# Kernel optimization log

Measured on AMD Instinct MI355X. Metric: run time of the kernel, lower is better.

## Reference

```python
import jax, jax.numpy as jnp
import numpy as np

LN2PI = float(np.log(2.0 * np.pi))
B, T, S = 256, 4096, 32


def setup_inputs() -> dict:
    key = jax.random.key(0)
    ks = jax.random.split(key, 6)
    obvs = jax.random.normal(ks[0], (B, T, 1), jnp.float32)
    ln_pi = jnp.ones((S,), jnp.float32) / S  # CategoricalPrior init: ones/num_states
    trans_w = 1.0 + 0.1 * jax.random.normal(ks[1], (S,), jnp.float32)  # diagonal
    trans_b = 0.1 * jax.random.normal(ks[2], (S,), jnp.float32)
    mu = jax.random.normal(ks[3], (S,), jnp.float32)
    log_sigma = 0.1 * jax.random.normal(ks[4], (S,), jnp.float32)
    return {"obvs": obvs, "ln_pi": ln_pi, "trans_w": trans_w,
            "trans_b": trans_b, "mu": mu, "log_sigma": log_sigma}


def reference(obvs, ln_pi, trans_w, trans_b, mu, log_sigma):
    # GaussianEmbedding: per-state Gaussian log-likelihood -> (B, T, S)
    z = (obvs - mu) * jnp.exp(-log_sigma)
    ln_e = -0.5 * z * z - log_sigma - 0.5 * LN2PI
    ln_e_t = jnp.swapaxes(ln_e, 0, 1)  # (T, B, S), time-major for scan

    # forward recurrence: f_t = emit_t + (w * f_{t-1} + b)
    f0 = ln_e_t[0] + ln_pi
    def fstep(carry, emit):
        nxt = emit + trans_w * carry + trans_b
        return nxt, nxt
    _, fs = jax.lax.scan(fstep, f0, ln_e_t[1:])
    ln_fs = jnp.concatenate([f0[None], fs], axis=0)  # (T, B, S)

    # backward recurrence: b_t = w * (b_{t+1} + emit_{t+1}) + b, b_{T-1} = emit_{T-1} + ln_pi
    bT = ln_e_t[-1] + ln_pi
    def bstep(carry, emit):
        nxt = trans_w * (carry + emit) + trans_b
        return nxt, nxt
    _, bs = jax.lax.scan(bstep, bT, ln_e_t[1:], reverse=True)  # bs[t] = b_t, t in [0, T-2]
    ln_bs = jnp.concatenate([bs, bT[None]], axis=0)  # (T, B, S)

    log_gamma = ln_fs + ln_bs
    log_gamma = log_gamma - jax.nn.logsumexp(log_gamma, axis=2, keepdims=True)
    return jnp.swapaxes(log_gamma, 0, 1)  # (B, T, S)
```

## Files before the change

kernel.cpp:

```cpp
#include <hip/hip_runtime.h>
#include <math.h>

constexpr int Bn = 256;
constexpr int Tn = 4096;
constexpr int Sn = 32;
constexpr int NE = 8;
constexpr int EL = Tn / NE;
constexpr int NT2 = 256;
constexpr int TCN = NT2 / Sn;
constexpr int TL = EL / TCN;
constexpr int CL = 16;
constexpr int CPT = TL / CL;
constexpr float HALF_LN2PI = 0.918938533204672742f;
constexpr float SAT = -3.0e38f;
constexpr float PCLAMP = 1.0e38f;

constexpr size_t OFF_LF = 0;
constexpr size_t OFF_LB = (size_t)Bn * NE * Sn;


#define DPP_ROR_ADD(x, ctrl) \
    ((x) + __int_as_float(__builtin_amdgcn_update_dpp(0, __float_as_int(x), (ctrl), 0xF, 0xF, false)))

__global__ __launch_bounds__(256) void hmm_agg_kernel(
    const float* __restrict__ obvs, const float* __restrict__ ln_pi,
    const float* __restrict__ trans_w, const float* __restrict__ trans_b,
    const float* __restrict__ mu, const float* __restrict__ log_sigma,
    float* __restrict__ ws)
{
    const int gid = blockIdx.x * 256 + threadIdx.x;
    const int s = gid & 31;
    const int e = (gid >> 5) & (NE - 1);
    const int b = gid >> 8;
    const float w  = trans_w[s];
    const float tb = trans_b[s];
    const float pi = ln_pi[s];
    const float m  = mu[s];
    const float ls = log_sigma[s];
    const float inv = __expf(-ls);
    const float cqa  = -0.5f * inv * inv;
    const float cqb  = m * inv * inv;
    const float cqcb = -ls - HALF_LN2PI - 0.5f * m * m * inv * inv + tb;
    const float tbb  = tb - w * tb;

    const float4* base = (const float4*)(obvs + (size_t)b * Tn + (size_t)e * EL);
    float a = 0.f, lb = 0.f;
#pragma unroll 4
    for (int j4 = 0; j4 < EL / 4; ++j4) {
        float4 x = base[j4];
        float4 y = base[EL / 4 - 1 - j4];
        float g0 = fmaf(fmaf(cqa, x.x, cqb), x.x, cqcb);
        float g1 = fmaf(fmaf(cqa, x.y, cqb), x.y, cqcb);
        float g2 = fmaf(fmaf(cqa, x.z, cqb), x.z, cqcb);
        float g3 = fmaf(fmaf(cqa, x.w, cqb), x.w, cqcb);
        if (e == 0 && j4 == 0) g0 += pi - tb;
        a = fmaf(w, a, g0);
        a = fmaf(w, a, g1);
        a = fmaf(w, a, g2);
        a = fmaf(w, a, g3);
        float d3 = fmaf(fmaf(cqa, y.w, cqb), y.w, cqcb);
        float d2 = fmaf(fmaf(cqa, y.z, cqb), y.z, cqcb);
        float d1 = fmaf(fmaf(cqa, y.y, cqb), y.y, cqcb);
        float d0 = fmaf(fmaf(cqa, y.x, cqb), y.x, cqcb);
        lb = fmaf(w, lb + d3, tbb);
        lb = fmaf(w, lb + d2, tbb);
        lb = fmaf(w, lb + d1, tbb);
        lb = fmaf(w, lb + d0, tbb);
    }
    ws[OFF_LF + (size_t)(b * NE + e) * Sn + s] = a;
    ws[OFF_LB + (size_t)(b * NE + e) * Sn + s] = lb;
}

__global__ __launch_bounds__(NT2, 8) void hmm_main_kernel(
    const float* __restrict__ obvs, const float* __restrict__ ln_pi,
    const float* __restrict__ trans_w, const float* __restrict__ trans_b,
    const float* __restrict__ mu, const float* __restrict__ log_sigma,
    float* __restrict__ out, const float* __restrict__ ws)
{
    __shared__ __align__(16) float s_obvs[EL];
    __shared__ float s_PF[TCN][Sn];
    __shared__ float s_ZB[TCN][Sn];
    __shared__ __align__(16) float s_tile[4][2][8][Sn];

    const int be  = blockIdx.x;
    const int b   = be >> 3;
    const int e   = be & (NE - 1);
    const int tid = threadIdx.x;
    const int s   = tid & 31;
    const int tc  = tid >> 5;
    const int wv  = tid >> 6;
    const int tcl = (tid >> 5) & 1;
    const int lane = tid & 63;
    const int t0  = tc * TL;

    if (tid < EL / 4)
        ((float4*)s_obvs)[tid] = ((const float4*)(obvs + (size_t)b * Tn + (size_t)e * EL))[tid];

    const float w  = trans_w[s];
    const float tb = trans_b[s];
    const float pi = ln_pi[s];
    const float m  = mu[s];
    const float ls = log_sigma[s];
    const float inv = __expf(-ls);
    const float cqa  = -0.5f * inv * inv;
    const float cqb  = m * inv * inv;
    const float cqcb = -ls - HALF_LN2PI - 0.5f * m * m * inv * inv + tb;
    const float tbb  = tb - w * tb;
    float w16; { float w2 = w * w, w4 = w2 * w2; float w8 = w4 * w4; w16 = w8 * w8; }
    const float W64 = fminf(fminf(w16 * w16, PCLAMP) * fminf(w16 * w16, PCLAMP), PCLAMP);
    const float l2w = log2f(w);
    const float WEL = fminf(exp2f(l2w * 512.0f), PCLAMP);
    const float pY  = fminf(exp2f(l2w * (float)(TL * tc)), PCLAMP);
    const float pX  = fminf(exp2f(l2w * (float)(TL * (7 - tc))), PCLAMP);
    const bool th0  = (e == 0) && (tc == 0);

    __syncthreads();

#define EMIT(xv) fmaf(fmaf(cqa, (xv), cqb), (xv), cqcb)

    float lbs[CPT];
    float AF = 0.f;
#pragma unroll
    for (int i = 0; i < CPT; ++i) {
        const float4* q4 = (const float4*)(s_obvs + t0 + i * CL);
        float4 v0 = q4[0], v1 = q4[1], v2 = q4[2], v3 = q4[3];
        float x[CL] = {v0.x, v0.y, v0.z, v0.w, v1.x, v1.y, v1.z, v1.w,
                       v2.x, v2.y, v2.z, v2.w, v3.x, v3.y, v3.z, v3.w};
#pragma unroll
        for (int j = 0; j < CL; ++j) {
            float g = EMIT(x[j]);
            if (th0 && i == 0 && j == 0) g += pi - tb;
            AF = fmaf(w, AF, g);
        }
        float l = 0.f;
#pragma unroll
        for (int j = CL - 2; j >= -1; --j)
            l = fmaf(w, l + EMIT(x[j + 1]), tbb);
        lbs[i] = l;
    }
    const float Z3 = lbs[3];
    const float Z2 = fmaf(w16, Z3, lbs[2]);
    const float Z1 = fmaf(w16, Z2, lbs[1]);
    const float ZT = fmaf(w16, Z1, lbs[0]);

    s_PF[tc][s] = AF;
    s_ZB[tc][s] = ZT;
    __syncthreads();

    {
        float Wd = W64;
#pragma unroll
        for (int r = 0; r < 3; ++r) {
            const int d = 1 << r;
            float tF = (tc >= d)      ? s_PF[tc - d][s] : 0.f;
            float tB = (tc + d < TCN) ? s_ZB[tc + d][s] : 0.f;
            __syncthreads();
            if (tc >= d)      s_PF[tc][s] = fmaf(Wd, tF, s_PF[tc][s]);
            if (tc + d < TCN) s_ZB[tc][s] = fmaf(Wd, tB, s_ZB[tc][s]);
            Wd = fminf(Wd * Wd, PCLAMP);
            __syncthreads();
        }
    }

    float Y = 0.f;
#pragma unroll
    for (int qq = 0; qq < NE - 1; ++qq)
        if (qq < e) Y = fmaf(WEL, Y, ws[OFF_LF + (size_t)(b * NE + qq) * Sn + s]);
    float xT = obvs[(size_t)b * Tn + Tn - 1];
    float X = EMIT(xT) + (pi - tb);
#pragma unroll
    for (int qq = NE - 1; qq > 0; --qq)
        if (qq > e) X = fmaf(WEL, X, ws[OFF_LB + (size_t)(b * NE + qq) * Sn + s]);

    const float Pprev  = (tc > 0)       ? s_PF[tc - 1][s] : 0.f;
    const float ZSnext = (tc < TCN - 1) ? s_ZB[tc + 1][s] : 0.f;
    float f         = fmaf(pY, Y, Pprev);
    const float Xth = fmaf(pX, X, ZSnext);
    float Rarr[CPT];
    Rarr[3] = Xth;
    {
        float p = w16;
        float Z = Z3;
        Rarr[2] = fmaf(p, Xth, Z);
        p = fminf(p * w16, PCLAMP); Z = Z2;
        Rarr[1] = fmaf(p, Xth, Z);
        p = fminf(p * w16, PCLAMP); Z = Z1;
        Rarr[0] = fmaf(p, Xth, Z);
    }

    const size_t rowbase = (size_t)b * Tn + (size_t)e * EL;
    const int qr  = lane & 7;
    const int t8r = (lane >> 3) & 7;

#pragma unroll
    for (int i = 0; i < CPT; ++i) {
        const float4* q4 = (const float4*)(s_obvs + t0 + i * CL);
        float4 v0 = q4[0], v1 = q4[1], v2 = q4[2], v3 = q4[3];
        float x[CL] = {v0.x, v0.y, v0.z, v0.w, v1.x, v1.y, v1.z, v1.w,
                       v2.x, v2.y, v2.z, v2.w, v3.x, v3.y, v3.z, v3.w};
        float barr[CL];
        barr[CL - 1] = Rarr[i];
#pragma unroll
        for (int j = CL - 2; j >= 0; --j)
            barr[j] = fmaf(w, barr[j + 1] + EMIT(x[j + 1]), tbb);

#pragma unroll
        for (int h = 0; h < 2; ++h) {
#pragma unroll
            for (int j8 = 0; j8 < 8; ++j8) {
                const int j = h * 8 + j8;
                float g = EMIT(x[j]);
                if (th0 && i == 0 && j == 0) g += pi - tb;
                f = fmaf(w, f, g);
                float v = f + barr[j];
                float sum = __expf(v);
                sum = DPP_ROR_ADD(sum, 0x121);
                sum = DPP_ROR_ADD(sum, 0x122);
                sum = DPP_ROR_ADD(sum, 0x124);
                sum = DPP_ROR_ADD(sum, 0x128);
                sum += __shfl_xor(sum, 16, 32);
                sum = fmaxf(sum, 1.0e-35f);
                s_tile[wv][tcl][j8][s] = fmaxf(v - __logf(sum), SAT);
            }
#pragma unroll
            for (int r2 = 0; r2 < 2; ++r2) {
                float4 val = *(const float4*)&s_tile[wv][r2][t8r][qr * 4];
                const int trow = (wv * 2 + r2) * TL + i * CL + h * 8 + t8r;
                *(float4*)(out + ((rowbase + trow) << 5) + qr * 4) = val;
            }
        }
    }
#undef EMIT
}

extern "C" void kernel_launch(void* const* d_in, const int* in_sizes, int n_in,
                              void* d_out, int out_size, void* d_ws, size_t ws_size,
                              hipStream_t stream)
{
    const float* obvs      = (const float*)d_in[0];
    const float* ln_pi     = (const float*)d_in[1];
    const float* trans_w   = (const float*)d_in[2];
    const float* trans_b   = (const float*)d_in[3];
    const float* mu        = (const float*)d_in[4];
    const float* log_sigma = (const float*)d_in[5];
    float* out = (float*)d_out;
    float* wsf = (float*)d_ws;

    hipLaunchKernelGGL(hmm_agg_kernel, dim3(Bn * NE * Sn / 256), dim3(256), 0, stream,
                       obvs, ln_pi, trans_w, trans_b, mu, log_sigma, wsf);
    hipLaunchKernelGGL(hmm_main_kernel, dim3(Bn * NE), dim3(NT2), 0, stream,
                       obvs, ln_pi, trans_w, trans_b, mu, log_sigma, out, wsf);
}
```

Measured before the change: 53.43 us.

## Precompute per-chunk scan prefixes in aggregate kernel and drop in-block scan

The aggregate kernel now also writes per-64-step forward prefix and backward suffix partials for each segment to the workspace. The main kernel reads them directly, which removes the shared-memory log-step scan and its barriers. Emissions are now computed once per element and reused by the forward and backward passes, and the cross-half-wave reduction uses permlane16_swap instead of a shuffle. The cost is more workspace traffic and stores in the first kernel, and the workspace must be large enough for the extra buffers.

After: 117.2 us. +119.4%, slower.

```diff
diff --git a/kernel.cpp b/kernel.cpp
--- a/kernel.cpp
+++ b/kernel.cpp
@@ -6,6 +6,7 @@
 constexpr int Sn = 32;
 constexpr int NE = 8;
 constexpr int EL = Tn / NE;
+constexpr int WPE = 8;
 constexpr int NT2 = 256;
 constexpr int TCN = NT2 / Sn;
 constexpr int TL = EL / TCN;
@@ -17,6 +18,8 @@
 
 constexpr size_t OFF_LF = 0;
 constexpr size_t OFF_LB = (size_t)Bn * NE * Sn;
+constexpr size_t OFF_PF = OFF_LB + (size_t)Bn * NE * Sn;
+constexpr size_t OFF_SB = OFF_PF + (size_t)Bn * NE * 7 * Sn;
 
 
 #define DPP_ROR_ADD(x, ctrl) \
@@ -45,27 +48,35 @@
 
     const float4* base = (const float4*)(obvs + (size_t)b * Tn + (size_t)e * EL);
     float a = 0.f, lb = 0.f;
-#pragma unroll 4
-    for (int j4 = 0; j4 < EL / 4; ++j4) {
-        float4 x = base[j4];
-        float4 y = base[EL / 4 - 1 - j4];
-        float g0 = fmaf(fmaf(cqa, x.x, cqb), x.x, cqcb);
-        float g1 = fmaf(fmaf(cqa, x.y, cqb), x.y, cqcb);
-        float g2 = fmaf(fmaf(cqa, x.z, cqb), x.z, cqcb);
-        float g3 = fmaf(fmaf(cqa, x.w, cqb), x.w, cqcb);
-        if (e == 0 && j4 == 0) g0 += pi - tb;
-        a = fmaf(w, a, g0);
-        a = fmaf(w, a, g1);
-        a = fmaf(w, a, g2);
-        a = fmaf(w, a, g3);
-        float d3 = fmaf(fmaf(cqa, y.w, cqb), y.w, cqcb);
-        float d2 = fmaf(fmaf(cqa, y.z, cqb), y.z, cqcb);
-        float d1 = fmaf(fmaf(cqa, y.y, cqb), y.y, cqcb);
-        float d0 = fmaf(fmaf(cqa, y.x, cqb), y.x, cqcb);
-        lb = fmaf(w, lb + d3, tbb);
-        lb = fmaf(w, lb + d2, tbb);
-        lb = fmaf(w, lb + d1, tbb);
-        lb = fmaf(w, lb + d0, tbb);
+#pragma unroll 1
+    for (int k = 0; k < WPE; ++k) {
+        const int kk = WPE - 1 - k;
+#pragma unroll 2
+        for (int j4 = 0; j4 < 16; ++j4) {
+            float4 x = base[k * 16 + j4];
+            float4 y = base[kk * 16 + (15 - j4)];
+            float g0 = fmaf(fmaf(cqa, x.x, cqb), x.x, cqcb);
+            float g1 = fmaf(fmaf(cqa, x.y, cqb), x.y, cqcb);
+            float g2 = fmaf(fmaf(cqa, x.z, cqb), x.z, cqcb);
+            float g3 = fmaf(fmaf(cqa, x.w, cqb), x.w, cqcb);
+            if (e == 0 && k == 0 && j4 == 0) g0 += pi - tb;
+            a = fmaf(w, a, g0);
+            a = fmaf(w, a, g1);
+            a = fmaf(w, a, g2);
+            a = fmaf(w, a, g3);
+            float d3 = fmaf(fmaf(cqa, y.w, cqb), y.w, cqcb);
+            float d2 = fmaf(fmaf(cqa, y.z, cqb), y.z, cqcb);
+            float d1 = fmaf(fmaf(cqa, y.y, cqb), y.y, cqcb);
+            float d0 = fmaf(fmaf(cqa, y.x, cqb), y.x, cqcb);
+            lb = fmaf(w, lb + d3, tbb);
+            lb = fmaf(w, lb + d2, tbb);
+            lb = fmaf(w, lb + d1, tbb);
+            lb = fmaf(w, lb + d0, tbb);
+        }
+        if (k < WPE - 1) {
+            ws[OFF_PF + ((size_t)(b * NE + e) * 7 + k) * Sn + s] = a;
+            ws[OFF_SB + ((size_t)(b * NE + e) * 7 + (kk - 1)) * Sn + s] = lb;
+        }
     }
     ws[OFF_LF + (size_t)(b * NE + e) * Sn + s] = a;
     ws[OFF_LB + (size_t)(b * NE + e) * Sn + s] = lb;
@@ -78,8 +89,6 @@
     float* __restrict__ out, const float* __restrict__ ws)
 {
     __shared__ __align__(16) float s_obvs[EL];
-    __shared__ float s_PF[TCN][Sn];
-    __shared__ float s_ZB[TCN][Sn];
     __shared__ __align__(16) float s_tile[4][2][8][Sn];
 
     const int be  = blockIdx.x;
@@ -107,7 +116,8 @@
     const float cqcb = -ls - HALF_LN2PI - 0.5f * m * m * inv * inv + tb;
     const float tbb  = tb - w * tb;
     float w16; { float w2 = w * w, w4 = w2 * w2; float w8 = w4 * w4; w16 = w8 * w8; }
-    const float W64 = fminf(fminf(w16 * w16, PCLAMP) * fminf(w16 * w16, PCLAMP), PCLAMP);
+    const float w32 = fminf(w16 * w16, PCLAMP);
+    const float w48 = fminf(w32 * w16, PCLAMP);
     const float l2w = log2f(w);
     const float WEL = fminf(exp2f(l2w * 512.0f), PCLAMP);
     const float pY  = fminf(exp2f(l2w * (float)(TL * tc)), PCLAMP);
@@ -118,8 +128,22 @@
 
 #define EMIT(xv) fmaf(fmaf(cqa, (xv), cqb), (xv), cqcb)
 
+    float Y = 0.f;
+#pragma unroll
+    for (int qq = 0; qq < NE - 1; ++qq)
+        if (qq < e) Y = fmaf(WEL, Y, ws[OFF_LF + (size_t)(b * NE + qq) * Sn + s]);
+    float xT = obvs[(size_t)b * Tn + Tn - 1];
+    float X = EMIT(xT) + (pi - tb);
+#pragma unroll
+    for (int qq = NE - 1; qq > 0; --qq)
+        if (qq > e) X = fmaf(WEL, X, ws[OFF_LB + (size_t)(b * NE + qq) * Sn + s]);
+
+    const float fprev = tc ? ws[OFF_PF + ((size_t)(b * NE + e) * 7 + (tc - 1)) * Sn + s] : 0.f;
+    float f = fmaf(pY, Y, fprev);
+    const float msuf = (tc < 7) ? ws[OFF_SB + ((size_t)(b * NE + e) * 7 + tc) * Sn + s] : 0.f;
+    const float Xth = fmaf(pX, X, msuf);
+
     float lbs[CPT];
-    float AF = 0.f;
 #pragma unroll
     for (int i = 0; i < CPT; ++i) {
         const float4* q4 = (const float4*)(s_obvs + t0 + i * CL);
@@ -127,66 +151,21 @@
         float x[CL] = {v0.x, v0.y, v0.z, v0.w, v1.x, v1.y, v1.z, v1.w,
                        v2.x, v2.y, v2.z, v2.w, v3.x, v3.y, v3.z, v3.w};
 #pragma unroll
-        for (int j = 0; j < CL; ++j) {
-            float g = EMIT(x[j]);
-            if (th0 && i == 0 && j == 0) g += pi - tb;
-            AF = fmaf(w, AF, g);
-        }
+        for (int j = 0; j < CL; ++j) x[j] = EMIT(x[j]);
         float l = 0.f;
 #pragma unroll
         for (int j = CL - 2; j >= -1; --j)
-            l = fmaf(w, l + EMIT(x[j + 1]), tbb);
+            l = fmaf(w, l + x[j + 1], tbb);
         lbs[i] = l;
     }
     const float Z3 = lbs[3];
     const float Z2 = fmaf(w16, Z3, lbs[2]);
     const float Z1 = fmaf(w16, Z2, lbs[1]);
-    const float ZT = fmaf(w16, Z1, lbs[0]);
-
-    s_PF[tc][s] = AF;
-    s_ZB[tc][s] = ZT;
-    __syncthreads();
-
-    {
-        float Wd = W64;
-#pragma unroll
-        for (int r = 0; r < 3; ++r) {
-            const int d = 1 << r;
-            float tF = (tc >= d)      ? s_PF[tc - d][s] : 0.f;
-            float tB = (tc + d < TCN) ? s_ZB[tc + d][s] : 0.f;
-            __syncthreads();
-            if (tc >= d)      s_PF[tc][s] = fmaf(Wd, tF, s_PF[tc][s]);
-            if (tc + d < TCN) s_ZB[tc][s] = fmaf(Wd, tB, s_ZB[tc][s]);
-            Wd = fminf(Wd * Wd, PCLAMP);
-            __syncthreads();
-        }
-    }
-
-    float Y = 0.f;
-#pragma unroll
-    for (int qq = 0; qq < NE - 1; ++qq)
-        if (qq < e) Y = fmaf(WEL, Y, ws[OFF_LF + (size_t)(b * NE + qq) * Sn + s]);
-    float xT = obvs[(size_t)b * Tn + Tn - 1];
-    float X = EMIT(xT) + (pi - tb);
-#pragma unroll
-    for (int qq = NE - 1; qq > 0; --qq)
-        if (qq > e) X = fmaf(WEL, X, ws[OFF_LB + (size_t)(b * NE + qq) * Sn + s]);
-
-    const float Pprev  = (tc > 0)       ? s_PF[tc - 1][s] : 0.f;
-    const float ZSnext = (tc < TCN - 1) ? s_ZB[tc + 1][s] : 0.f;
-    float f         = fmaf(pY, Y, Pprev);
-    const float Xth = fmaf(pX, X, ZSnext);
     float Rarr[CPT];
     Rarr[3] = Xth;
-    {
-        float p = w16;
-        float Z = Z3;
-        Rarr[2] = fmaf(p, Xth, Z);
-        p = fminf(p * w16, PCLAMP); Z = Z2;
-        Rarr[1] = fmaf(p, Xth, Z);
-        p = fminf(p * w16, PCLAMP); Z = Z1;
-        Rarr[0] = fmaf(p, Xth, Z);
-    }
+    Rarr[2] = fmaf(w16, Xth, Z3);
+    Rarr[1] = fmaf(w32, Xth, Z2);
+    Rarr[0] = fmaf(w48, Xth, Z1);
 
     const size_t rowbase = (size_t)b * Tn + (size_t)e * EL;
     const int qr  = lane & 7;
@@ -198,27 +177,33 @@
         float4 v0 = q4[0], v1 = q4[1], v2 = q4[2], v3 = q4[3];
         float x[CL] = {v0.x, v0.y, v0.z, v0.w, v1.x, v1.y, v1.z, v1.w,
                        v2.x, v2.y, v2.z, v2.w, v3.x, v3.y, v3.z, v3.w};
+#pragma unroll
+        for (int j = 0; j < CL; ++j) x[j] = EMIT(x[j]);
+        if (th0 && i == 0) x[0] += pi - tb;
+
         float barr[CL];
         barr[CL - 1] = Rarr[i];
 #pragma unroll
         for (int j = CL - 2; j >= 0; --j)
-            barr[j] = fmaf(w, barr[j + 1] + EMIT(x[j + 1]), tbb);
+            barr[j] = fmaf(w, barr[j + 1] + x[j + 1], tbb);
 
 #pragma unroll
         for (int h = 0; h < 2; ++h) {
 #pragma unroll
             for (int j8 = 0; j8 < 8; ++j8) {
                 const int j = h * 8 + j8;
-                float g = EMIT(x[j]);
-                if (th0 && i == 0 && j == 0) g += pi - tb;
-                f = fmaf(w, f, g);
+                f = fmaf(w, f, x[j]);
                 float v = f + barr[j];
                 float sum = __expf(v);
                 sum = DPP_ROR_ADD(sum, 0x121);
                 sum = DPP_ROR_ADD(sum, 0x122);
                 sum = DPP_ROR_ADD(sum, 0x124);
                 sum = DPP_ROR_ADD(sum, 0x128);
-                sum += __shfl_xor(sum, 16, 32);
+                {
+                    auto r = __builtin_amdgcn_permlane16_swap(
+                        __float_as_uint(sum), __float_as_uint(sum), false, false);
+                    sum = __uint_as_float(r[0]) + __uint_as_float(r[1]);
+                }
                 sum = fmaxf(sum, 1.0e-35f);
                 s_tile[wv][tcl][j8][s] = fmaxf(v - __logf(sum), SAT);
             }
```

## Parallelize chunk aggregation kernel across time sub-chunks with shared-memory scan

Applied to the files above, without the earlier changes.

The aggregation kernel previously ran one thread per (batch, chunk, state), walking 512 timesteps serially and reading obvs straight from global memory. It now uses 256-thread blocks per (batch, chunk). Each block stages obvs in shared memory, computes 64-step partial forward and backward aggregates per thread group, and combines them with a log-step Hillis-Steele scan over 8 groups. This shortens the serial dependency chain by spreading it over more threads. In exchange it adds shared-memory traffic and several __syncthreads. The main kernel also swaps the serial power chain for precomputed w32/w48 constants.

Result: faster. 47.75 us (-10.6%).

```diff
diff --git a/kernel.cpp b/kernel.cpp
--- a/kernel.cpp
+++ b/kernel.cpp
@@ -22,65 +22,15 @@
 #define DPP_ROR_ADD(x, ctrl) \
     ((x) + __int_as_float(__builtin_amdgcn_update_dpp(0, __float_as_int(x), (ctrl), 0xF, 0xF, false)))
 
-__global__ __launch_bounds__(256) void hmm_agg_kernel(
+__global__ __launch_bounds__(NT2, 8) void hmm_agg_kernel(
     const float* __restrict__ obvs, const float* __restrict__ ln_pi,
     const float* __restrict__ trans_w, const float* __restrict__ trans_b,
     const float* __restrict__ mu, const float* __restrict__ log_sigma,
     float* __restrict__ ws)
 {
-    const int gid = blockIdx.x * 256 + threadIdx.x;
-    const int s = gid & 31;
-    const int e = (gid >> 5) & (NE - 1);
-    const int b = gid >> 8;
-    const float w  = trans_w[s];
-    const float tb = trans_b[s];
-    const float pi = ln_pi[s];
-    const float m  = mu[s];
-    const float ls = log_sigma[s];
-    const float inv = __expf(-ls);
-    const float cqa  = -0.5f * inv * inv;
-    const float cqb  = m * inv * inv;
-    const float cqcb = -ls - HALF_LN2PI - 0.5f * m * m * inv * inv + tb;
-    const float tbb  = tb - w * tb;
-
-    const float4* base = (const float4*)(obvs + (size_t)b * Tn + (size_t)e * EL);
-    float a = 0.f, lb = 0.f;
-#pragma unroll 4
-    for (int j4 = 0; j4 < EL / 4; ++j4) {
-        float4 x = base[j4];
-        float4 y = base[EL / 4 - 1 - j4];
-        float g0 = fmaf(fmaf(cqa, x.x, cqb), x.x, cqcb);
-        float g1 = fmaf(fmaf(cqa, x.y, cqb), x.y, cqcb);
-        float g2 = fmaf(fmaf(cqa, x.z, cqb), x.z, cqcb);
-        float g3 = fmaf(fmaf(cqa, x.w, cqb), x.w, cqcb);
-        if (e == 0 && j4 == 0) g0 += pi - tb;
-        a = fmaf(w, a, g0);
-        a = fmaf(w, a, g1);
-        a = fmaf(w, a, g2);
-        a = fmaf(w, a, g3);
-        float d3 = fmaf(fmaf(cqa, y.w, cqb), y.w, cqcb);
-        float d2 = fmaf(fmaf(cqa, y.z, cqb), y.z, cqcb);
-        float d1 = fmaf(fmaf(cqa, y.y, cqb), y.y, cqcb);
-        float d0 = fmaf(fmaf(cqa, y.x, cqb), y.x, cqcb);
-        lb = fmaf(w, lb + d3, tbb);
-        lb = fmaf(w, lb + d2, tbb);
-        lb = fmaf(w, lb + d1, tbb);
-        lb = fmaf(w, lb + d0, tbb);
-    }
-    ws[OFF_LF + (size_t)(b * NE + e) * Sn + s] = a;
-    ws[OFF_LB + (size_t)(b * NE + e) * Sn + s] = lb;
-}
-
-__global__ __launch_bounds__(NT2, 8) void hmm_main_kernel(
-    const float* __restrict__ obvs, const float* __restrict__ ln_pi,
-    const float* __restrict__ trans_w, const float* __restrict__ trans_b,
-    const float* __restrict__ mu, const float* __restrict__ log_sigma,
-    float* __restrict__ out, const float* __restrict__ ws)
-{
     __shared__ __align__(16) float s_obvs[EL];
     __shared__ float s_PF[TCN][Sn];
     __shared__ float s_ZB[TCN][Sn];
-    __shared__ __align__(16) float s_tile[4][2][8][Sn];
 
     const int be  = blockIdx.x;
     const int b   = be >> 3;
@@ -88,9 +38,6 @@
     const int tid = threadIdx.x;
     const int s   = tid & 31;
     const int tc  = tid >> 5;
-    const int wv  = tid >> 6;
-    const int tcl = (tid >> 5) & 1;
-    const int lane = tid & 63;
     const int t0  = tc * TL;
 
     if (tid < EL / 4)
@@ -107,7 +54,102 @@
     const float cqcb = -ls - HALF_LN2PI - 0.5f * m * m * inv * inv + tb;
     const float tbb  = tb - w * tb;
     float w16; { float w2 = w * w, w4 = w2 * w2; float w8 = w4 * w4; w16 = w8 * w8; }
-    const float W64 = fminf(fminf(w16 * w16, PCLAMP) * fminf(w16 * w16, PCLAMP), PCLAMP);
+    const float w32 = fminf(w16 * w16, PCLAMP);
+    const float W64 = fminf(w32 * w32, PCLAMP);
+    const bool th0  = (e == 0) && (tc == 0);
+
+    __syncthreads();
+
+#define EMIT(xv) fmaf(fmaf(cqa, (xv), cqb), (xv), cqcb)
+
+    float lbs[CPT];
+    float AF = 0.f;
+#pragma unroll
+    for (int i = 0; i < CPT; ++i) {
+        const float4* q4 = (const float4*)(s_obvs + t0 + i * CL);
+        float4 v0 = q4[0], v1 = q4[1], v2 = q4[2], v3 = q4[3];
+        float x[CL] = {v0.x, v0.y, v0.z, v0.w, v1.x, v1.y, v1.z, v1.w,
+                       v2.x, v2.y, v2.z, v2.w, v3.x, v3.y, v3.z, v3.w};
+#pragma unroll
+        for (int j = 0; j < CL; ++j) {
+            float g = EMIT(x[j]);
+            if (th0 && i == 0 && j == 0) g += pi - tb;
+            AF = fmaf(w, AF, g);
+        }
+        float l = 0.f;
+#pragma unroll
+        for (int j = CL - 2; j >= -1; --j)
+            l = fmaf(w, l + EMIT(x[j + 1]), tbb);
+        lbs[i] = l;
+    }
+    const float Z3 = lbs[3];
+    const float Z2 = fmaf(w16, Z3, lbs[2]);
+    const float Z1 = fmaf(w16, Z2, lbs[1]);
+    const float ZT = fmaf(w16, Z1, lbs[0]);
+
+    s_PF[tc][s] = AF;
+    s_ZB[tc][s] = ZT;
+    __syncthreads();
+
+    {
+        float Wd = W64;
+#pragma unroll
+        for (int r = 0; r < 3; ++r) {
+            const int d = 1 << r;
+            float tF = (tc >= d)      ? s_PF[tc - d][s] : 0.f;
+            float tB = (tc + d < TCN) ? s_ZB[tc + d][s] : 0.f;
+            __syncthreads();
+            if (tc >= d)      s_PF[tc][s] = fmaf(Wd, tF, s_PF[tc][s]);
+            if (tc + d < TCN) s_ZB[tc][s] = fmaf(Wd, tB, s_ZB[tc][s]);
+            Wd = fminf(Wd * Wd, PCLAMP);
+            __syncthreads();
+        }
+    }
+
+    if (tc == 7) ws[OFF_LF + (size_t)be * Sn + s] = s_PF[TCN - 1][s];
+    if (tc == 0) ws[OFF_LB + (size_t)be * Sn + s] = s_ZB[0][s];
+#undef EMIT
+}
+
+__global__ __launch_bounds__(NT2, 8) void hmm_main_kernel(
+    const float* __restrict__ obvs, const float* __restrict__ ln_pi,
+    const float* __restrict__ trans_w, const float* __restrict__ trans_b,
+    const float* __restrict__ mu, const float* __restrict__ log_sigma,
+    float* __restrict__ out, const float* __restrict__ ws)
+{
+    __shared__ __align__(16) float s_obvs[EL];
+    __shared__ float s_PF[TCN][Sn];
+    __shared__ float s_ZB[TCN][Sn];
+    __shared__ __align__(16) float s_tile[4][2][8][Sn];
+
+    const int be  = blockIdx.x;
+    const int b   = be >> 3;
+    const int e   = be & (NE - 1);
+    const int tid = threadIdx.x;
+    const int s   = tid & 31;
+    const int tc  = tid >> 5;
+    const int wv  = tid >> 6;
+    const int tcl = (tid >> 5) & 1;
+    const int lane = tid & 63;
+    const int t0  = tc * TL;
+
+    if (tid < EL / 4)
+        ((float4*)s_obvs)[tid] = ((const float4*)(obvs + (size_t)b * Tn + (size_t)e * EL))[tid];
+
+    const float w  = trans_w[s];
+    const float tb = trans_b[s];
+    const float pi = ln_pi[s];
+    const float m  = mu[s];
+    const float ls = log_sigma[s];
+    const float inv = __expf(-ls);
+    const float cqa  = -0.5f * inv * inv;
+    const float cqb  = m * inv * inv;
+    const float cqcb = -ls - HALF_LN2PI - 0.5f * m * m * inv * inv + tb;
+    const float tbb  = tb - w * tb;
+    float w16; { float w2 = w * w, w4 = w2 * w2; float w8 = w4 * w4; w16 = w8 * w8; }
+    const float w32 = fminf(w16 * w16, PCLAMP);
+    const float w48 = fminf(w32 * w16, PCLAMP);
+    const float W64 = fminf(w32 * w32, PCLAMP);
     const float l2w = log2f(w);
     const float WEL = fminf(exp2f(l2w * 512.0f), PCLAMP);
     const float pY  = fminf(exp2f(l2w * (float)(TL * tc)), PCLAMP);
@@ -178,15 +220,9 @@
     const float Xth = fmaf(pX, X, ZSnext);
     float Rarr[CPT];
     Rarr[3] = Xth;
-    {
-        float p = w16;
-        float Z = Z3;
-        Rarr[2] = fmaf(p, Xth, Z);
-        p = fminf(p * w16, PCLAMP); Z = Z2;
-        Rarr[1] = fmaf(p, Xth, Z);
-        p = fminf(p * w16, PCLAMP); Z = Z1;
-        Rarr[0] = fmaf(p, Xth, Z);
-    }
+    Rarr[2] = fmaf(w16, Xth, Z3);
+    Rarr[1] = fmaf(w32, Xth, Z2);
+    Rarr[0] = fmaf(w48, Xth, Z1);
 
     const size_t rowbase = (size_t)b * Tn + (size_t)e * EL;
     const int qr  = lane & 7;
@@ -246,7 +282,7 @@
     float* out = (float*)d_out;
     float* wsf = (float*)d_ws;
 
-    hipLaunchKernelGGL(hmm_agg_kernel, dim3(Bn * NE * Sn / 256), dim3(256), 0, stream,
+    hipLaunchKernelGGL(hmm_agg_kernel, dim3(Bn * NE), dim3(NT2), 0, stream,
                        obvs, ln_pi, trans_w, trans_b, mu, log_sigma, wsf);
     hipLaunchKernelGGL(hmm_main_kernel, dim3(Bn * NE), dim3(NT2), 0, stream,
                        obvs, ln_pi, trans_w, trans_b, mu, log_sigma, out, wsf);
```
